# Performance work log

Measured on AMD Instinct MI355X. Metric: run time of the kernel, lower is better.

The kernel has to match this reference:

```python
import jax, jax.numpy as jnp
import numpy as np

NH = 1024
VS = 50257
CUT0 = 1675          # round(VS/30)
CUT1 = 3 * CUT0      # 5025
N_CLUSTERS = 2
HEAD_SIZE = CUT0 + N_CLUSTERS          # 1677
D0, D1 = NH // 4, NH // 16             # 256, 64
SZ0, SZ1 = CUT1 - CUT0, VS - CUT1      # 3350, 45232


def setup_inputs() -> dict:
    key = jax.random.key(0)
    ks = jax.random.split(key, 8)
    s = 0.02
    return {
        "x": jax.random.normal(ks[0], (8, 512, NH), dtype=jnp.float32),
        "y": jax.random.randint(ks[1], (8, 512), 0, VS, dtype=jnp.int64),
        "head_w": jax.random.normal(ks[2], (HEAD_SIZE, NH), dtype=jnp.float32) * s,
        "head_b": jnp.zeros((HEAD_SIZE,), dtype=jnp.float32),
        "proj0": jax.random.normal(ks[3], (D0, NH), dtype=jnp.float32) * s,
        "w0": jax.random.normal(ks[4], (SZ0, D0), dtype=jnp.float32) * s,
        "proj1": jax.random.normal(ks[5], (D1, NH), dtype=jnp.float32) * s,
        "w1": jax.random.normal(ks[6], (SZ1, D1), dtype=jnp.float32) * s,
    }


def reference(x, y, head_w, head_b, proj0, w0, proj1, w1):
    # Flatten as in the torch forward: x -> [N, nh], y -> [N]
    xf = x.reshape(-1, x.shape[-1])            # [N, NH]
    yf = y.reshape(-1)                         # [N]

    # Head: shortlist tokens + 2 cluster logits
    head_logits = jnp.einsum('nh,vh->nv', xf, head_w) + head_b   # [N, 1677]
    head_lp = jax.nn.log_softmax(head_logits, axis=-1)

    # Default: target in head shortlist
    in_head = yf < CUT0
    idx_head = jnp.where(in_head, yf, 0)
    out = jnp.take_along_axis(head_lp, idx_head[:, None], axis=1)[:, 0]

    # Tail clusters: dense per-cluster small GEMMs + log-softmax, masked select
    for i, (low, high, proj, w) in enumerate(
            [(CUT0, CUT1, proj0, w0), (CUT1, VS, proj1, w1)]):
        size = high - low
        h = jnp.einsum('nh,dh->nd', xf, proj)          # [N, d_i]
        lp = jax.nn.log_softmax(jnp.einsum('nd,vd->nv', h, w), axis=-1)  # [N, size]
        rel = jnp.clip(yf - low, 0, size - 1)
        cl = head_lp[:, CUT0 + i] + jnp.take_along_axis(lp, rel[:, None], axis=1)[:, 0]
        mask = (yf >= low) & (yf < high)
        out = jnp.where(mask, cl, out)

    loss = -jnp.mean(out)
    return out, loss
```

## Files before the change

kernel.cpp:

```cpp
#include <hip/hip_runtime.h>
#include <stdint.h>

#define NROWS 4096
#define NHID 1024
#define CC0 1675
#define CC1 5025
#define HEADSZ 1677
#define PD0 256
#define PD1 64
#define TSZ0 3350
#define TSZ1 45232
#define HPN (HEADSZ + PD0 + PD1)
#define TPC1 6
#define L2E 1.4426950408889634f
#define LN2 0.6931471805599453f

#define NB_HD 448
#define NB_PJ 96
#define NB_CW 512
#define NB_MID (NB_HD + NB_PJ + NB_CW)

#define NB_C1 1888
#define NB_C0 864
#define NB_TG 1024
#define NB_TAIL (NB_C1 + NB_C0 + NB_TG)

typedef __attribute__((ext_vector_type(8))) __bf16 bf16x8;
typedef __attribute__((ext_vector_type(4))) float f32x4;

__device__ __forceinline__ unsigned short f2bf(float f) {
  union { float f; uint32_t u; } v; v.f = f;
  return (unsigned short)((v.u + 0x7FFFu + ((v.u >> 16) & 1u)) >> 16);
}
__device__ __forceinline__ float bfl(uint32_t u) {
  union { uint32_t u; float f; } v; v.u = u << 16; return v.f;
}
__device__ __forceinline__ float bfh(uint32_t u) {
  union { uint32_t u; float f; } v; v.u = u & 0xFFFF0000u; return v.f;
}
__device__ __forceinline__ float bf1(unsigned short u) {
  union { uint32_t u; float f; } v; v.u = ((uint32_t)u) << 16; return v.f;
}
#define EXP2(x) __builtin_amdgcn_exp2f(x)

#define CV1 1048576
#define CV2 1477888
#define CV3 1543424
#define CV4 1559808
#define CV5 1774208
#define CV6 2497920
#define CVW0 (CV5 - CV4)
#define CVW  (CV6 - CV4)

__global__ void conv_part(const float* __restrict__ x, const float* __restrict__ hw,
                          const float* __restrict__ p0, const float* __restrict__ p1,
                          unsigned short* __restrict__ dst,
                          const int* __restrict__ y,
                          int* __restrict__ idx0, int* __restrict__ pos0,
                          int* __restrict__ idx1, int* __restrict__ pos1,
                          int* __restrict__ n01) {
  if (blockIdx.x == 1024) {
    __shared__ int sc0[256], sc1[256], nsh[2];
    int t = threadIdx.x;
    int yl[16];
    int c0 = 0, c1 = 0;
#pragma unroll
    for (int k = 0; k < 16; ++k) {
      int yv = y[t * 16 + k];
      yl[k] = yv;
      c0 += (yv >= CC0 && yv < CC1);
      c1 += (yv >= CC1);
    }
    sc0[t] = c0; sc1[t] = c1;
    __syncthreads();
    if (t == 0) {
      int a0 = 0, a1 = 0;
      for (int i = 0; i < 256; ++i) {
        int v0 = sc0[i]; sc0[i] = a0; a0 += v0;
        int v1 = sc1[i]; sc1[i] = a1; a1 += v1;
      }
      n01[0] = a0; n01[1] = a1; nsh[0] = a0; nsh[1] = a1;
    }
    __syncthreads();
    int p0c = sc0[t], p1c = sc1[t];
#pragma unroll
    for (int k = 0; k < 16; ++k) {
      int n = t * 16 + k, yv = yl[k];
      if (yv >= CC0 && yv < CC1) { idx0[p0c] = n; pos0[n] = p0c; ++p0c; }
      else if (yv >= CC1)        { idx1[p1c] = n; pos1[n] = p1c; ++p1c; }
    }
    for (int j = nsh[0] + t; j < NROWS; j += 256) idx0[j] = 0;
    for (int j = nsh[1] + t; j < NROWS; j += 256) idx1[j] = 0;
    return;
  }
  const int stride = 1024 * 256;
  for (int i = blockIdx.x * 256 + threadIdx.x; i < CV4; i += stride) {
    const float* src; int off; float sc;
    if (i < CV1)      { src = x;  off = i;       sc = 1.f; }
    else if (i < CV2) { src = hw; off = i - CV1; sc = L2E; }
    else if (i < CV3) { src = p0; off = i - CV2; sc = 1.f; }
    else              { src = p1; off = i - CV3; sc = 1.f; }
    float4 v = reinterpret_cast<const float4*>(src)[off];
    ushort4 o;
    o.x = f2bf(v.x * sc); o.y = f2bf(v.y * sc);
    o.z = f2bf(v.z * sc); o.w = f2bf(v.w * sc);
    reinterpret_cast<ushort4*>(dst)[i] = o;
  }
}

#define GLOAD(g, l) __builtin_amdgcn_global_load_lds( \
    (const __attribute__((address_space(1))) uint32_t*)(const void*)(g), \
    (__attribute__((address_space(3))) uint32_t*)(void*)(l), 16, 0, 0)

#define SWZB(L) ((L) ^ ((((L) >> 7) & 7) << 4))

__device__ __forceinline__
void gemm_core(const unsigned short* __restrict__ A, int lda,
               const unsigned short* __restrict__ B, int ldb,
               int N, int K, int tile0, int tile1, int brow,
               const float* __restrict__ bias,
               float* __restrict__ sum_out,
               unsigned short* __restrict__ Cout, int ldc, int coutStart,
               unsigned short* AsB, unsigned short* BsB,
               const int* __restrict__ gidx) {
  const int tid = threadIdx.x;
  const int lane = tid & 63;
  const int wid = tid >> 6;
  const int wrow = (wid >> 1) * 64;
  const int wcol = (wid & 1) * 64;
  const int lr = lane & 15, lg = lane >> 4;
  const int nsteps = (tile1 - tile0) * (K >> 5);
  const int rowBase = brow + wrow;

  int arowc[2];
#pragma unroll
  for (int c = 0; c < 2; ++c) {
    int g = wid * 128 + c * 64 + lane;
    int S = SWZB(g * 16);
    int row = S >> 6;
    arowc[c] = gidx ? gidx[brow + row] : brow + row;
  }

  float sacc[4][4];
#pragma unroll
  for (int m = 0; m < 4; ++m)
#pragma unroll
    for (int r = 0; r < 4; ++r) sacc[m][r] = 0.f;

  auto stage = [&](int b, int tt, int kk) {
#pragma unroll
    for (int c = 0; c < 2; ++c) {
      int g = wid * 128 + c * 64 + lane;
      int L = g * 16;
      int S = SWZB(L);
      int row = S >> 6, ko = (S >> 4) & 3;
      GLOAD(A + (size_t)arowc[c] * lda + kk + ko * 8, (char*)AsB + b * 8192 + L);
      int bsrc = tt * 128 + row; bsrc = bsrc < N ? bsrc : N - 1;
      GLOAD(B + (size_t)bsrc * ldb + kk + ko * 8, (char*)BsB + b * 8192 + L);
    }
  };

  f32x4 acc[4][4];
#pragma unroll
  for (int m = 0; m < 4; ++m)
#pragma unroll
    for (int n = 0; n < 4; ++n) acc[m][n] = (f32x4){0.f, 0.f, 0.f, 0.f};

  int tp = tile0, kp = 0;
  auto adv = [&](int& t, int& k) { k += 32; if (k == K) { k = 0; ++t; } };
  stage(0, tp, kp); adv(tp, kp);
  if (nsteps > 1) { stage(1, tp, kp); adv(tp, kp); }

  int tile = tile0, k0 = 0;
  for (int s = 0; s < nsteps; ++s) {
    if (s + 1 < nsteps) asm volatile("s_waitcnt vmcnt(4)" ::: "memory");
    else                asm volatile("s_waitcnt vmcnt(0)" ::: "memory");
    __builtin_amdgcn_s_barrier();
    if (s + 2 < nsteps) { stage((s + 2) % 3, tp, kp); adv(tp, kp); }

    const int cur = s % 3;
    int k0n = k0 + 32, tn = tile;
    if (k0n == K) { k0n = 0; tn = tile + 1; }

    bf16x8 af[4], bfv[4];
#pragma unroll
    for (int m = 0; m < 4; ++m)
      af[m] = *(const bf16x8*)((const char*)AsB + cur * 8192 +
                               SWZB((wrow + m * 16 + lr) * 64 + lg * 16));
#pragma unroll
    for (int n = 0; n < 4; ++n)
      bfv[n] = *(const bf16x8*)((const char*)BsB + cur * 8192 +
                                SWZB((wcol + n * 16 + lr) * 64 + lg * 16));
#pragma unroll
    for (int m = 0; m < 4; ++m)
#pragma unroll
      for (int n = 0; n < 4; ++n)
        acc[m][n] = __builtin_amdgcn_mfma_f32_16x16x32_bf16(af[m], bfv[n], acc[m][n], 0, 0, 0);

    if (tn != tile) {
      const int cb = tile * 128 + wcol;
#pragma unroll
      for (int m = 0; m < 4; ++m)
#pragma unroll
        for (int n = 0; n < 4; ++n) {
#pragma unroll
          for (int r = 0; r < 4; ++r) {
            int col = cb + n * 16 + lr;
            if (col < N) {
              float v = acc[m][n][r];
              if (Cout && col >= coutStart) {
                int row = rowBase + m * 16 + lg * 4 + r;
                Cout[(size_t)row * ldc + (col - coutStart)] = f2bf(v);
              } else {
                if (bias) v = fmaf(bias[col], L2E, v);
                sacc[m][r] += EXP2(v);
              }
            }
          }
          acc[m][n] = (f32x4){0.f, 0.f, 0.f, 0.f};
        }
    }
    tile = tn; k0 = k0n;
  }

#pragma unroll
  for (int m = 0; m < 4; ++m)
#pragma unroll
    for (int r = 0; r < 4; ++r) {
      float s = sacc[m][r];
      s += __shfl_xor(s, 1); s += __shfl_xor(s, 2);
      s += __shfl_xor(s, 4); s += __shfl_xor(s, 8);
      if (lr == 0) atomicAdd(&sum_out[rowBase + m * 16 + lg * 4 + r], s);
    }
}

__device__ __forceinline__
void gemm_core2(const unsigned short* __restrict__ A, int lda,
                const unsigned short* __restrict__ B, int ldb,
                int N, int K, int tile0, int brow,
                const float* __restrict__ bias,
                float* __restrict__ sum_out,
                unsigned short* __restrict__ Cout, int ldc, int coutStart,
                char* AsB, char* BsB) {
  const int tid = threadIdx.x;
  const int lane = tid & 63;
  const int wid = tid >> 6;
  const int wrow = (wid >> 1) * 64;
  const int wcol = (wid & 1) * 64;
  const int lr = lane & 15, lg = lane >> 4;
  const int nsteps = K >> 6;
  const int rowBase = brow + wrow;

  auto stage = [&](int b, int kk) {
#pragma unroll
    for (int c = 0; c < 4; ++c) {
      int L = (c * 256 + tid) * 16;
      int kh = L >> 13;
      int L8 = L & 8191;
      int S = SWZB(L8);
      int row = S >> 6, ko = (S >> 4) & 3;
      int koff = kk + kh * 32 + ko * 8;
      GLOAD(A + (size_t)(brow + row) * lda + koff, AsB + b * 16384 + L);
      int bsrc = tile0 * 128 + row; bsrc = bsrc < N ? bsrc : N - 1;
      GLOAD(B + (size_t)bsrc * ldb + koff, BsB + b * 16384 + L);
    }
  };

  f32x4 acc[4][4];
#pragma unroll
  for (int m = 0; m < 4; ++m)
#pragma unroll
    for (int n = 0; n < 4; ++n) acc[m][n] = (f32x4){0.f, 0.f, 0.f, 0.f};

  stage(0, 0);
  asm volatile("s_waitcnt vmcnt(0)" ::: "memory");
  __builtin_amdgcn_s_barrier();

  for (int s = 0; s < nsteps; ++s) {
    if (s + 1 < nsteps) stage((s + 1) & 1, (s + 1) * 64);
    const int cur = s & 1;
#pragma unroll
    for (int kh = 0; kh < 2; ++kh) {
      bf16x8 af[4], bfv[4];
#pragma unroll
      for (int m = 0; m < 4; ++m)
        af[m] = *(const bf16x8*)(AsB + cur * 16384 + kh * 8192 +
                                 SWZB((wrow + m * 16 + lr) * 64 + lg * 16));
#pragma unroll
      for (int n = 0; n < 4; ++n)
        bfv[n] = *(const bf16x8*)(BsB + cur * 16384 + kh * 8192 +
                                  SWZB((wcol + n * 16 + lr) * 64 + lg * 16));
#pragma unroll
      for (int m = 0; m < 4; ++m)
#pragma unroll
        for (int n = 0; n < 4; ++n)
          acc[m][n] = __builtin_amdgcn_mfma_f32_16x16x32_bf16(af[m], bfv[n], acc[m][n], 0, 0, 0);
    }
    if (s + 1 < nsteps) {
      asm volatile("s_waitcnt vmcnt(0)" ::: "memory");
      __builtin_amdgcn_s_barrier();
    }
  }

  const int cb = tile0 * 128 + wcol;
  float sacc[4][4];
#pragma unroll
  for (int m = 0; m < 4; ++m)
#pragma unroll
    for (int r = 0; r < 4; ++r) sacc[m][r] = 0.f;
#pragma unroll
  for (int m = 0; m < 4; ++m)
#pragma unroll
    for (int n = 0; n < 4; ++n)
#pragma unroll
      for (int r = 0; r < 4; ++r) {
        int col = cb + n * 16 + lr;
        if (col < N) {
          float v = acc[m][n][r];
          if (Cout && col >= coutStart) {
            int row = rowBase + m * 16 + lg * 4 + r;
            Cout[(size_t)row * ldc + (col - coutStart)] = f2bf(v);
          } else {
            if (bias) v = fmaf(bias[col], L2E, v);
            sacc[m][r] += EXP2(v);
          }
        }
      }
  if (sum_out) {
#pragma unroll
    for (int m = 0; m < 4; ++m)
#pragma unroll
      for (int r = 0; r < 4; ++r) {
        float s = sacc[m][r];
        s += __shfl_xor(s, 1); s += __shfl_xor(s, 2);
        s += __shfl_xor(s, 4); s += __shfl_xor(s, 8);
        if (lr == 0) atomicAdd(&sum_out[rowBase + m * 16 + lg * 4 + r], s);
      }
  }
}

__global__ __launch_bounds__(256, 2)
void fused_mid(const unsigned short* __restrict__ xb,
               const unsigned short* __restrict__ hpb,
               const float* __restrict__ head_b,
               float* __restrict__ hs,
               unsigned short* __restrict__ hb,
               const float* __restrict__ w0f, const float* __restrict__ w1f,
               unsigned short* __restrict__ dstAll) {
  __shared__ __align__(16) char lds[65536];
  const int bid = blockIdx.x;

  if (bid < NB_HD) {
    const int xcd = bid & 7;
    const int local = bid >> 3;
    const int rowBlk = xcd * 4 + local / 14;
    const int colChunk = local % 14;
    gemm_core2(xb, NHID, hpb, NHID, HEADSZ, NHID, colChunk, rowBlk * 128,
               head_b, hs, nullptr, 0, 0, lds, lds + 32768);
    return;
  }

  if (bid < NB_HD + NB_PJ) {
    const int b1 = bid - NB_HD;
    const int cpx = NB_PJ >> 3;
    const int sid = (b1 & 7) * cpx + (b1 >> 3);
    const int rowBlk = sid & 31;
    const int colChunk = sid >> 5;
    gemm_core2(xb, NHID, hpb + (size_t)HEADSZ * NHID, NHID, PD0 + PD1, NHID,
               colChunk, rowBlk * 128,
               nullptr, nullptr, hb, PD0 + PD1, 0, lds, lds + 32768);
    return;
  }

  {
    const int b2 = bid - NB_HD - NB_PJ;
    const int stride = NB_CW * 256;
    for (int i = b2 * 256 + (int)threadIdx.x; i < CVW; i += stride) {
      const float* src; int off;
      if (i < CVW0) { src = w0f; off = i; }
      else          { src = w1f; off = i - CVW0; }
      float4 v = reinterpret_cast<const float4*>(src)[off];
      ushort4 o;
      o.x = f2bf(v.x * L2E); o.y = f2bf(v.y * L2E);
      o.z = f2bf(v.z * L2E); o.w = f2bf(v.w * L2E);
      reinterpret_cast<ushort4*>(dstAll)[CV4 + i] = o;
    }
  }
}

__global__ __launch_bounds__(256, 3)
void fused_tail(const unsigned short* __restrict__ hb,
                const unsigned short* __restrict__ w0b,
                const unsigned short* __restrict__ w1b,
                const unsigned short* __restrict__ xb,
                const unsigned short* __restrict__ hwb,
                const float* __restrict__ head_b,
                const int* __restrict__ y,
                const int* __restrict__ idx0, const int* __restrict__ idx1,
                const int* __restrict__ n01,
                float* __restrict__ s0, float* __restrict__ s1,
                float* __restrict__ ht, float* __restrict__ tc) {
  __shared__ __align__(16) unsigned short lds[6 * 4096];
  const int bid = blockIdx.x;

  if (bid < NB_C1) {
    const int tid = threadIdx.x;
    const int lane = tid & 63;
    const int wid = tid >> 6;
    const int lr = lane & 15, lg = lane >> 4;
    const int cpx = NB_C1 >> 3;
    const int sid = (bid & 7) * cpx + (bid >> 3);
    const int rowBlk = sid & 31;
    const int colChunk = sid >> 5;
    if (rowBlk * 128 >= n01[1]) return;
    const int rowBase = rowBlk * 128 + (wid >> 1) * 64;
    const int wcol = (wid & 1) * 64;
    const int tile0 = colChunk * TPC1;

    int colOff[4], srcOff[4];
#pragma unroll
    for (int c = 0; c < 4; ++c) {
      int L = (c * 256 + tid) * 16;
      int S = L ^ (((L >> 7) & 7) << 4);
      colOff[c] = S >> 7;
      srcOff[c] = (S & 127) >> 1;
    }
    auto stage = [&](int b, int t) {
#pragma unroll
      for (int c = 0; c < 4; ++c) {
        int gc = t * 128 + colOff[c];
        gc = gc < TSZ1 ? gc : TSZ1 - 1;
        GLOAD(w1b + (size_t)gc * PD1 + srcOff[c],
              (char*)lds + b * 16384 + (c * 256 + tid) * 16);
      }
    };

    bf16x8 af[4][2];
#pragma unroll
    for (int m = 0; m < 4; ++m) {
      int ridx = idx1[rowBase + m * 16 + lr];
      const unsigned short* p = hb + PD0 +
          (size_t)ridx * (PD0 + PD1) + lg * 8;
      af[m][0] = *(const bf16x8*)p;
      af[m][1] = *(const bf16x8*)(p + 32);
    }

    float sacc[4][4];
#pragma unroll
    for (int m = 0; m < 4; ++m)
#pragma unroll
      for (int r = 0; r < 4; ++r) sacc[m][r] = 0.f;

    stage(0, tile0);
    stage(1, tile0 + 1);

#pragma unroll 1
    for (int s = 0; s < TPC1; ++s) {
      if (s + 1 < TPC1) asm volatile("s_waitcnt vmcnt(4)" ::: "memory");
      else              asm volatile("s_waitcnt vmcnt(0)" ::: "memory");
      __builtin_amdgcn_s_barrier();
      if (s + 2 < TPC1) stage((s + 2) % 3, tile0 + s + 2);

      const int cur = s % 3;
      const int cb = (tile0 + s) * 128 + wcol;
      const int full = (cb + 63 < TSZ1);

#pragma unroll
      for (int nh = 0; nh < 2; ++nh) {
        bf16x8 bf[2][2];
#pragma unroll
        for (int nn = 0; nn < 2; ++nn) {
          int ccol = wcol + (nh * 2 + nn) * 16 + lr;
#pragma unroll
          for (int kh = 0; kh < 2; ++kh) {
            int L = ccol * 128 + kh * 64 + lg * 16;
            bf[nn][kh] = *(const bf16x8*)((const char*)lds + cur * 16384 +
                                          (L ^ ((ccol & 7) << 4)));
          }
        }
        f32x4 acc[4][2];
#pragma unroll
        for (int m = 0; m < 4; ++m)
#pragma unroll
          for (int nn = 0; nn < 2; ++nn) {
            f32x4 a = (f32x4){0.f, 0.f, 0.f, 0.f};
            a = __builtin_amdgcn_mfma_f32_16x16x32_bf16(af[m][0], bf[nn][0], a, 0, 0, 0);
            a = __builtin_amdgcn_mfma_f32_16x16x32_bf16(af[m][1], bf[nn][1], a, 0, 0, 0);
            acc[m][nn] = a;
          }
        if (full) {
#pragma unroll
          for (int m = 0; m < 4; ++m)
#pragma unroll
            for (int r = 0; r < 4; ++r)
              sacc[m][r] += EXP2(acc[m][0][r]) + EXP2(acc[m][1][r]);
        } else {
#pragma unroll
          for (int m = 0; m < 4; ++m)
#pragma unroll
            for (int r = 0; r < 4; ++r) {
              float t = 0.f;
#pragma unroll
              for (int nn = 0; nn < 2; ++nn)
                if (cb + (nh * 2 + nn) * 16 + lr < TSZ1) t += EXP2(acc[m][nn][r]);
              sacc[m][r] += t;
            }
        }
      }
    }

#pragma unroll
    for (int m = 0; m < 4; ++m)
#pragma unroll
      for (int r = 0; r < 4; ++r) {
        float s = sacc[m][r];
        s += __shfl_xor(s, 1); s += __shfl_xor(s, 2);
        s += __shfl_xor(s, 4); s += __shfl_xor(s, 8);
        if (lr == 0) atomicAdd(&s1[rowBase + m * 16 + lg * 4 + r], s);
      }
    return;
  }

  if (bid < NB_C1 + NB_C0) {
    const int b0 = bid - NB_C1;
    const int cpx = NB_C0 >> 3;
    const int sid = (b0 & 7) * cpx + (b0 >> 3);
    const int rowBlk = sid & 31;
    const int colChunk = sid >> 5;
    if (rowBlk * 128 >= n01[0]) return;
    gemm_core(hb, PD0 + PD1, w0b, PD0, TSZ0, PD0, colChunk, colChunk + 1,
              rowBlk * 128, nullptr, s0, nullptr, 0, 0,
              (unsigned short*)lds, (unsigned short*)lds + 3 * 4096, idx0);
    return;
  }

  {
    const int b2 = bid - NB_C1 - NB_C0;
    int row = b2 * 4 + (threadIdx.x >> 6);
    int lane = threadIdx.x & 63;
    int yv = y[row];
    int th = yv < CC0 ? yv : (yv < CC1 ? CC0 : CC0 + 1);

    const unsigned short* xr = xb + (size_t)row * NHID + lane * 16;
    const unsigned short* wr = hwb + (size_t)th * NHID + lane * 16;
    uint4 xa = *(const uint4*)xr,       wa = *(const uint4*)wr;
    uint4 xc = *(const uint4*)(xr + 8), wc = *(const uint4*)(wr + 8);
    float s = 0.f;
    uint32_t xs[8] = {xa.x, xa.y, xa.z, xa.w, xc.x, xc.y, xc.z, xc.w};
    uint32_t ws[8] = {wa.x, wa.y, wa.z, wa.w, wc.x, wc.y, wc.z, wc.w};
#pragma unroll
    for (int j = 0; j < 8; ++j)
      s += bfl(xs[j]) * bfl(ws[j]) + bfh(xs[j]) * bfh(ws[j]);
#pragma unroll
    for (int d = 1; d < 64; d <<= 1) s += __shfl_xor(s, d);

    float cl = 0.f;
    if (yv >= CC0) {
      if (yv < CC1) {
        int rel = yv - CC0;
        const unsigned short* hr = hb + (size_t)row * (PD0 + PD1) + lane * 4;
        const unsigned short* w0r = w0b + (size_t)rel * PD0 + lane * 4;
        uint2 ha = *(const uint2*)hr, wa0 = *(const uint2*)w0r;
        cl = bfl(ha.x) * bfl(wa0.x) + bfh(ha.x) * bfh(wa0.x)
           + bfl(ha.y) * bfl(wa0.y) + bfh(ha.y) * bfh(wa0.y);
      } else {
        int rel = yv - CC1;
        cl = bf1(hb[(size_t)row * (PD0 + PD1) + PD0 + lane])
           * bf1(w1b[(size_t)rel * PD1 + lane]);
      }
#pragma unroll
      for (int d = 1; d < 64; d <<= 1) cl += __shfl_xor(cl, d);
    }
    if (lane == 0) { ht[row] = s * LN2 + head_b[th]; tc[row] = (yv < CC0) ? 0.f : cl; }
  }
}

__global__ void rowloss(const float* __restrict__ hs, const float* __restrict__ ht,
                        const float* __restrict__ s0, const float* __restrict__ s1,
                        const float* __restrict__ tc,
                        const int* __restrict__ pos0, const int* __restrict__ pos1,
                        const int* __restrict__ y, float* __restrict__ out) {
  int n = blockIdx.x * 256 + threadIdx.x;
  int yv = y[n];
  float o = ht[n] - __builtin_amdgcn_logf(hs[n]) * LN2;
  if (yv >= CC0) {
    float sv = (yv < CC1) ? s0[pos0[n]] : s1[pos1[n]];
    o += tc[n] * LN2 - __builtin_amdgcn_logf(sv) * LN2;
  }
  out[n] = o;
  float l = o;
#pragma unroll
  for (int d = 1; d < 64; d <<= 1) l += __shfl_xor(l, d);
  __shared__ float red[4];
  if ((threadIdx.x & 63) == 0) red[threadIdx.x >> 6] = l;
  __syncthreads();
  if (threadIdx.x == 0)
    atomicAdd(&out[NROWS], -(red[0] + red[1] + red[2] + red[3]) / (float)NROWS);
}

extern "C" void kernel_launch(void* const* d_in, const int* in_sizes, int n_in,
                              void* d_out, int out_size, void* d_ws, size_t ws_size,
                              hipStream_t stream) {
  const float* x      = (const float*)d_in[0];
  const int*   y      = (const int*)d_in[1];
  const float* head_w = (const float*)d_in[2];
  const float* head_b = (const float*)d_in[3];
  const float* proj0  = (const float*)d_in[4];
  const float* w0     = (const float*)d_in[5];
  const float* proj1  = (const float*)d_in[6];
  const float* w1     = (const float*)d_in[7];
  float* out = (float*)d_out;

  char* wp = (char*)d_ws;
  unsigned short* xb  = (unsigned short*)wp; wp += (size_t)NROWS * NHID * 2;
  unsigned short* hpb = (unsigned short*)wp; wp += (size_t)HPN * NHID * 2;
  unsigned short* w0b = (unsigned short*)wp; wp += (size_t)TSZ0 * PD0 * 2;
  unsigned short* w1b = (unsigned short*)wp; wp += (size_t)TSZ1 * PD1 * 2;
  unsigned short* hb  = (unsigned short*)wp; wp += (size_t)NROWS * (PD0 + PD1) * 2;
  float* hs = (float*)wp; wp += NROWS * 4;
  float* s0 = (float*)wp; wp += NROWS * 4;
  float* s1 = (float*)wp; wp += NROWS * 4;
  float* ht = (float*)wp; wp += NROWS * 4;
  float* tc = (float*)wp; wp += NROWS * 4;
  int* idx0 = (int*)wp; wp += NROWS * 4;
  int* pos0 = (int*)wp; wp += NROWS * 4;
  int* idx1 = (int*)wp; wp += NROWS * 4;
  int* pos1 = (int*)wp; wp += NROWS * 4;
  int* n01  = (int*)wp; wp += 8 * 4;

  hipMemsetAsync(hs, 0, 3 * NROWS * 4, stream);
  hipMemsetAsync(out + NROWS, 0, 4, stream);

  conv_part<<<dim3(1025), 256, 0, stream>>>(
      x, head_w, proj0, proj1, xb, y, idx0, pos0, idx1, pos1, n01);

  fused_mid<<<dim3(NB_MID), 256, 0, stream>>>(
      xb, hpb, head_b, hs, hb, w0, w1, xb);

  fused_tail<<<dim3(NB_TAIL), 256, 0, stream>>>(
      hb, w0b, w1b, xb, hpb, head_b, y, idx0, idx1, n01, s0, s1, ht, tc);

  rowloss<<<dim3(NROWS / 256), 256, 0, stream>>>(
      hs, ht, s0, s1, tc, pos0, pos1, y, out);
}
```

Before: 102.9 us.

## Halve GEMM row tile in fused_mid and fold memsets into conversion kernel

The head and projection GEMMs in fused_mid now use 64-row tiles instead of 128-row tiles. This doubles the block counts, shrinks LDS to 48KB and raises launch bounds to 3 blocks per CU, aiming for better occupancy and load balance. The two hipMemsetAsync calls are replaced by seven extra blocks in conv_part that zero the accumulators, which saves separate launches. Smaller tiles mean less reuse of the B operand and more redundant loads of head weights.

```diff
diff --git a/kernel.cpp b/kernel.cpp
--- a/kernel.cpp
+++ b/kernel.cpp
@@ -15,8 +15,8 @@
 #define L2E 1.4426950408889634f
 #define LN2 0.6931471805599453f
 
-#define NB_HD 448
-#define NB_PJ 96
+#define NB_HD 896
+#define NB_PJ 192
 #define NB_CW 512
 #define NB_MID (NB_HD + NB_PJ + NB_CW)
 
@@ -58,7 +58,15 @@
                           const int* __restrict__ y,
                           int* __restrict__ idx0, int* __restrict__ pos0,
                           int* __restrict__ idx1, int* __restrict__ pos1,
-                          int* __restrict__ n01) {
+                          int* __restrict__ n01,
+                          float* __restrict__ hs3, float* __restrict__ outp) {
+  if (blockIdx.x >= 1025) {
+    int z = blockIdx.x - 1025;
+    for (int i = z * 256 + (int)threadIdx.x; i < 3 * NROWS; i += 7 * 256)
+      hs3[i] = 0.f;
+    if (z == 0 && threadIdx.x == 0) outp[NROWS] = 0.f;
+    return;
+  }
   if (blockIdx.x == 1024) {
     __shared__ int sc0[256], sc1[256], nsh[2];
     int t = threadIdx.x;
@@ -235,17 +243,17 @@
 }
 
 __device__ __forceinline__
-void gemm_core2(const unsigned short* __restrict__ A, int lda,
+void gemm_core3(const unsigned short* __restrict__ A, int lda,
                 const unsigned short* __restrict__ B, int ldb,
                 int N, int K, int tile0, int brow,
                 const float* __restrict__ bias,
                 float* __restrict__ sum_out,
-                unsigned short* __restrict__ Cout, int ldc, int coutStart,
+                unsigned short* __restrict__ Cout, int ldc,
                 char* AsB, char* BsB) {
   const int tid = threadIdx.x;
   const int lane = tid & 63;
   const int wid = tid >> 6;
-  const int wrow = (wid >> 1) * 64;
+  const int wrow = (wid >> 1) * 32;
   const int wcol = (wid & 1) * 64;
   const int lr = lane & 15, lg = lane >> 4;
   const int nsteps = K >> 6;
@@ -253,22 +261,29 @@
 
   auto stage = [&](int b, int kk) {
 #pragma unroll
-    for (int c = 0; c < 4; ++c) {
-      int L = (c * 256 + tid) * 16;
-      int kh = L >> 13;
-      int L8 = L & 8191;
-      int S = SWZB(L8);
-      int row = S >> 6, ko = (S >> 4) & 3;
-      int koff = kk + kh * 32 + ko * 8;
-      GLOAD(A + (size_t)(brow + row) * lda + koff, AsB + b * 16384 + L);
-      int bsrc = tile0 * 128 + row; bsrc = bsrc < N ? bsrc : N - 1;
-      GLOAD(B + (size_t)bsrc * ldb + koff, BsB + b * 16384 + L);
+    for (int kh = 0; kh < 2; ++kh) {
+      {
+        int L4 = tid * 16;
+        int S = SWZB(L4);
+        int row = S >> 6, ko = (S >> 4) & 3;
+        GLOAD(A + (size_t)(brow + row) * lda + kk + kh * 32 + ko * 8,
+              AsB + b * 8192 + kh * 4096 + L4);
+      }
+#pragma unroll
+      for (int c = 0; c < 2; ++c) {
+        int L8 = (c * 256 + tid) * 16;
+        int S = SWZB(L8);
+        int col = S >> 6, ko = (S >> 4) & 3;
+        int bsrc = tile0 * 128 + col; bsrc = bsrc < N ? bsrc : N - 1;
+        GLOAD(B + (size_t)bsrc * ldb + kk + kh * 32 + ko * 8,
+              BsB + b * 16384 + kh * 8192 + L8);
+      }
     }
   };
 
-  f32x4 acc[4][4];
-#pragma unroll
-  for (int m = 0; m < 4; ++m)
+  f32x4 acc[2][4];
+#pragma unroll
+  for (int m = 0; m < 2; ++m)
 #pragma unroll
     for (int n = 0; n < 4; ++n) acc[m][n] = (f32x4){0.f, 0.f, 0.f, 0.f};
 
@@ -281,17 +296,17 @@
     const int cur = s & 1;
 #pragma unroll
     for (int kh = 0; kh < 2; ++kh) {
-      bf16x8 af[4], bfv[4];
-#pragma unroll
-      for (int m = 0; m < 4; ++m)
-        af[m] = *(const bf16x8*)(AsB + cur * 16384 + kh * 8192 +
+      bf16x8 af[2], bfv[4];
+#pragma unroll
+      for (int m = 0; m < 2; ++m)
+        af[m] = *(const bf16x8*)(AsB + cur * 8192 + kh * 4096 +
                                  SWZB((wrow + m * 16 + lr) * 64 + lg * 16));
 #pragma unroll
       for (int n = 0; n < 4; ++n)
         bfv[n] = *(const bf16x8*)(BsB + cur * 16384 + kh * 8192 +
                                   SWZB((wcol + n * 16 + lr) * 64 + lg * 16));
 #pragma unroll
-      for (int m = 0; m < 4; ++m)
+      for (int m = 0; m < 2; ++m)
 #pragma unroll
         for (int n = 0; n < 4; ++n)
           acc[m][n] = __builtin_amdgcn_mfma_f32_16x16x32_bf16(af[m], bfv[n], acc[m][n], 0, 0, 0);
@@ -303,13 +318,13 @@
   }
 
   const int cb = tile0 * 128 + wcol;
-  float sacc[4][4];
-#pragma unroll
-  for (int m = 0; m < 4; ++m)
+  float sacc[2][4];
+#pragma unroll
+  for (int m = 0; m < 2; ++m)
 #pragma unroll
     for (int r = 0; r < 4; ++r) sacc[m][r] = 0.f;
 #pragma unroll
-  for (int m = 0; m < 4; ++m)
+  for (int m = 0; m < 2; ++m)
 #pragma unroll
     for (int n = 0; n < 4; ++n)
 #pragma unroll
@@ -317,9 +332,9 @@
         int col = cb + n * 16 + lr;
         if (col < N) {
           float v = acc[m][n][r];
-          if (Cout && col >= coutStart) {
+          if (Cout) {
             int row = rowBase + m * 16 + lg * 4 + r;
-            Cout[(size_t)row * ldc + (col - coutStart)] = f2bf(v);
+            Cout[(size_t)row * ldc + col] = f2bf(v);
           } else {
             if (bias) v = fmaf(bias[col], L2E, v);
             sacc[m][r] += EXP2(v);
@@ -328,7 +343,7 @@
       }
   if (sum_out) {
 #pragma unroll
-    for (int m = 0; m < 4; ++m)
+    for (int m = 0; m < 2; ++m)
 #pragma unroll
       for (int r = 0; r < 4; ++r) {
         float s = sacc[m][r];
@@ -339,7 +354,7 @@
   }
 }
 
-__global__ __launch_bounds__(256, 2)
+__global__ __launch_bounds__(256, 3)
 void fused_mid(const unsigned short* __restrict__ xb,
                const unsigned short* __restrict__ hpb,
                const float* __restrict__ head_b,
@@ -347,16 +362,16 @@
                unsigned short* __restrict__ hb,
                const float* __restrict__ w0f, const float* __restrict__ w1f,
                unsigned short* __restrict__ dstAll) {
-  __shared__ __align__(16) char lds[65536];
+  __shared__ __align__(16) char lds[49152];
   const int bid = blockIdx.x;
 
   if (bid < NB_HD) {
     const int xcd = bid & 7;
     const int local = bid >> 3;
-    const int rowBlk = xcd * 4 + local / 14;
+    const int rowBlk = xcd * 8 + local / 14;
     const int colChunk = local % 14;
-    gemm_core2(xb, NHID, hpb, NHID, HEADSZ, NHID, colChunk, rowBlk * 128,
-               head_b, hs, nullptr, 0, 0, lds, lds + 32768);
+    gemm_core3(xb, NHID, hpb, NHID, HEADSZ, NHID, colChunk, rowBlk * 64,
+               head_b, hs, nullptr, 0, lds, lds + 16384);
     return;
   }
 
@@ -364,11 +379,11 @@
     const int b1 = bid - NB_HD;
     const int cpx = NB_PJ >> 3;
     const int sid = (b1 & 7) * cpx + (b1 >> 3);
-    const int rowBlk = sid & 31;
-    const int colChunk = sid >> 5;
-    gemm_core2(xb, NHID, hpb + (size_t)HEADSZ * NHID, NHID, PD0 + PD1, NHID,
-               colChunk, rowBlk * 128,
-               nullptr, nullptr, hb, PD0 + PD1, 0, lds, lds + 32768);
+    const int rowBlk = sid & 63;
+    const int colChunk = sid >> 6;
+    gemm_core3(xb, NHID, hpb + (size_t)HEADSZ * NHID, NHID, PD0 + PD1, NHID,
+               colChunk, rowBlk * 64,
+               nullptr, nullptr, hb, PD0 + PD1, lds, lds + 16384);
     return;
   }
 
@@ -628,11 +643,8 @@
   int* pos1 = (int*)wp; wp += NROWS * 4;
   int* n01  = (int*)wp; wp += 8 * 4;
 
-  hipMemsetAsync(hs, 0, 3 * NROWS * 4, stream);
-  hipMemsetAsync(out + NROWS, 0, 4, stream);
-
-  conv_part<<<dim3(1025), 256, 0, stream>>>(
-      x, head_w, proj0, proj1, xb, y, idx0, pos0, idx1, pos1, n01);
+  conv_part<<<dim3(1032), 256, 0, stream>>>(
+      x, head_w, proj0, proj1, xb, y, idx0, pos0, idx1, pos1, n01, hs, out);
 
   fused_mid<<<dim3(NB_MID), 256, 0, stream>>>(
       xb, hpb, head_b, hs, hb, w0, w1, xb);
```

New measurement: 97.79 us. 5.0% less time.
